# Optimization experiments

Hardware: AMD Instinct MI355X
Metric: run time of the kernel (lower is better)

The kernel has to match this reference:

```python
import jax, jax.numpy as jnp
import numpy as np

EPS = 1e-5

def setup_inputs() -> dict:
    key = jax.random.key(0)
    k1, k2 = jax.random.split(key)
    N, D = 8192, 256
    q_features = jax.random.normal(k1, (N, D), dtype=jnp.float32)
    g_features = jax.random.normal(k2, (N, D), dtype=jnp.float32)
    return {"q_features": q_features, "g_features": g_features}

def reference(q_features, g_features):
    # logits[i, j] = q_i . g_j ; original computes row i as g_features @ q_i
    logits = jnp.einsum('id,jd->ij', q_features, g_features)  # [N, N]
    # exp(l_ii)/sum_j exp(l_ij) == softmax row diagonal (stable form, same math)
    probs_diag = jnp.diagonal(jax.nn.softmax(logits, axis=-1))  # [N]
    loss = jnp.mean(-jnp.log(probs_diag + EPS))
    return loss
```

## Files before the change

kernel.cpp:

```cpp
#include <hip/hip_runtime.h>
#include <stdint.h>


#define LOG2E 1.44269504f
#define KOFF  92.3324826f

typedef __attribute__((ext_vector_type(4))) float f32x4;
typedef long long i64;

typedef __attribute__((address_space(1))) const uint32_t gu32;
typedef __attribute__((address_space(3))) uint32_t lu32;

__global__ __launch_bounds__(256) void k_cvt(const float* __restrict__ q,
                                             const float* __restrict__ g,
                                             char* __restrict__ qb,
                                             char* __restrict__ gb) {
    int o = blockIdx.x * 256 + threadIdx.x;
    const float* src = q;
    char* dst = qb;
    float sc = LOG2E;
    if (o >= 262144) { o -= 262144; src = g; dst = gb; sc = 1.0f; }
    int row = o >> 5, slot = o & 31;
    int ks = slot >> 2, quad = slot & 3;
    const float4* sp = (const float4*)(src + row * 256 + slot * 8);
    float4 a = sp[0], b = sp[1];
    uint32_t w0 = __builtin_amdgcn_cvt_pk_fp8_f32(a.x * sc, a.y * sc, 0, false);
    w0 = __builtin_amdgcn_cvt_pk_fp8_f32(a.z * sc, a.w * sc, w0, true);
    uint32_t w1 = __builtin_amdgcn_cvt_pk_fp8_f32(b.x * sc, b.y * sc, 0, false);
    w1 = __builtin_amdgcn_cvt_pk_fp8_f32(b.z * sc, b.w * sc, w1, true);
    int p = row >> 6, cf = (row >> 4) & 3, l15 = row & 15;
    uint2 wv; wv.x = w0; wv.y = w1;
    *(uint2*)(dst + (size_t)p * 16384 + (ks * 4 + cf) * 512 + (quad * 16 + l15) * 8) = wv;
}

__global__ __launch_bounds__(256, 2) void k_main(const char* __restrict__ qb,
                                                 const char* __restrict__ gb,
                                                 float* __restrict__ zpart,
                                                 float* __restrict__ diag) {
    __shared__ char lds[16384];
    const int tid  = threadIdx.x;
    const int wave = tid >> 6;
    const int lane = tid & 63;
    const int l15  = lane & 15;
    const int quad = lane >> 4;
    const int t    = blockIdx.x >> 5;
    const int cs   = blockIdx.x & 31;
    const int rowbase = t * 256 + wave * 64;

    i64 afrag[4][8];
    {
        const char* qp = qb + (size_t)(t * 4 + wave) * 16384 + lane * 8;
#pragma unroll
        for (int rg = 0; rg < 4; ++rg)
#pragma unroll
            for (int ks = 0; ks < 8; ++ks)
                afrag[rg][ks] = *(const i64*)(qp + ((ks * 4 + rg) << 9));
    }

    float zacc[4][4];
#pragma unroll
    for (int rg = 0; rg < 4; ++rg)
#pragma unroll
        for (int r = 0; r < 4; ++r) zacc[rg][r] = 0.f;

    const bool bd = (t == cs);

    for (int jt = 0; jt < 4; ++jt) {
        const char* gp = gb + (size_t)(cs * 4 + jt) * 16384;
#pragma unroll
        for (int i = 0; i < 4; ++i) {
            int c = wave * 4 + i;
            __builtin_amdgcn_global_load_lds(
                (gu32*)(gp + (c << 10) + (lane << 4)),
                (lu32*)(lds + (c << 10)), 16, 0, 0);
        }
        __syncthreads();

        const bool dg = bd && (jt == wave);
#pragma unroll
        for (int cf = 0; cf < 4; ++cf) {
            f32x4 acc[4];
#pragma unroll
            for (int rg = 0; rg < 4; ++rg)
                acc[rg] = (f32x4){-KOFF, -KOFF, -KOFF, -KOFF};
#pragma unroll
            for (int ks = 0; ks < 8; ++ks) {
                i64 b = *(const i64*)(lds + ((ks * 4 + cf) << 9) + lane * 8);
#pragma unroll
                for (int rg = 0; rg < 4; ++rg)
                    acc[rg] = __builtin_amdgcn_mfma_f32_16x16x32_fp8_fp8(
                        afrag[rg][ks], b, acc[rg], 0, 0, 0);
            }
#pragma unroll
            for (int rg = 0; rg < 4; ++rg)
#pragma unroll
                for (int r = 0; r < 4; ++r)
                    zacc[rg][r] += __builtin_amdgcn_exp2f(acc[rg][r]);
            if (dg) {
#pragma unroll
                for (int r = 0; r < 4; ++r)
                    if (quad * 4 + r == l15)
                        diag[rowbase + cf * 16 + l15] = acc[cf][r];
            }
        }
        __syncthreads();
    }

#pragma unroll
    for (int d = 1; d < 16; d <<= 1)
#pragma unroll
        for (int rg = 0; rg < 4; ++rg)
#pragma unroll
            for (int r = 0; r < 4; ++r)
                zacc[rg][r] += __shfl_xor(zacc[rg][r], d, 64);

    if (l15 == 0) {
#pragma unroll
        for (int rg = 0; rg < 4; ++rg)
#pragma unroll
            for (int r = 0; r < 4; ++r)
                zpart[(rowbase + rg * 16 + quad * 4 + r) * 32 + cs] = zacc[rg][r];
    }
}

__global__ __launch_bounds__(256) void k_fin1(const float* __restrict__ zpart,
                                              const float* __restrict__ diag,
                                              float* __restrict__ partial) {
    __shared__ float red[4];
    int r = blockIdx.x * 256 + threadIdx.x;
    const float4* z = (const float4*)(zpart + r * 32);
    float Z = 0.f;
#pragma unroll
    for (int i = 0; i < 8; ++i) {
        float4 a = z[i];
        Z += (a.x + a.y) + (a.z + a.w);
    }
    float p = __builtin_amdgcn_exp2f(diag[r]) / Z;
    float v = -logf(p + 1e-5f);
#pragma unroll
    for (int dd = 1; dd < 64; dd <<= 1) v += __shfl_xor(v, dd, 64);
    if ((threadIdx.x & 63) == 0) red[threadIdx.x >> 6] = v;
    __syncthreads();
    if (threadIdx.x == 0)
        partial[blockIdx.x] = (red[0] + red[1]) + (red[2] + red[3]);
}

__global__ void k_fin2(const float* __restrict__ partial, float* __restrict__ out) {
    float v = (threadIdx.x < 32) ? partial[threadIdx.x] : 0.f;
#pragma unroll
    for (int d = 1; d < 32; d <<= 1) v += __shfl_xor(v, d, 64);
    if (threadIdx.x == 0) out[0] = v * (1.f / 8192.f);
}

extern "C" void kernel_launch(void* const* d_in, const int* in_sizes, int n_in,
                              void* d_out, int out_size, void* d_ws, size_t ws_size,
                              hipStream_t stream) {
    const float* q = (const float*)d_in[0];
    const float* g = (const float*)d_in[1];
    char* ws = (char*)d_ws;
    char*  qb     = ws;
    char*  gb     = ws + (2u << 20);
    float* diag   = (float*)(ws + (4u << 20));
    float* zpart  = (float*)(ws + (4u << 20) + (32u << 10));
    float* partial= (float*)(ws + (4u << 20) + (1056u << 10));
    k_cvt <<<2048, 256, 0, stream>>>(q, g, qb, gb);
    k_main<<<1024, 256, 0, stream>>>(qb, gb, zpart, diag);
    k_fin1<<<32,   256, 0, stream>>>(zpart, diag, partial);
    k_fin2<<<1,     64, 0, stream>>>(partial, (float*)d_out);
    (void)in_sizes; (void)n_in; (void)out_size; (void)ws_size;
}
```

Baseline: 97.25 us.

## Switch to 16x16x128 scaled FP8 MFMA with repacked operand layout

Replaces the 16x16x32 FP8 MFMA with the gfx950 scaled 16x16x128 f8f6f4 MFMA using unit scales (0x7f). The conversion kernel's output layout changes so each lane loads 32 contiguous-K bytes as two 16-byte pieces, and LDS and A-fragment loads become 128-bit reads. This cuts MFMA instruction count by four and halves load instruction count per K. The risk is that the K ordering inside the new operand must match between the A and B sides, and that the wider vectors raise register pressure.

```diff
diff --git a/kernel.cpp b/kernel.cpp
--- a/kernel.cpp
+++ b/kernel.cpp
@@ -6,10 +6,18 @@
 #define KOFF  92.3324826f
 
 typedef __attribute__((ext_vector_type(4))) float f32x4;
-typedef long long i64;
+typedef __attribute__((ext_vector_type(4))) int   i32x4;
+typedef __attribute__((ext_vector_type(8))) int   i32x8;
 
 typedef __attribute__((address_space(1))) const uint32_t gu32;
 typedef __attribute__((address_space(3))) uint32_t lu32;
+
+static __device__ __forceinline__ i32x8 cat8(i32x4 lo, i32x4 hi) {
+    i32x8 r;
+    r[0] = lo[0]; r[1] = lo[1]; r[2] = lo[2]; r[3] = lo[3];
+    r[4] = hi[0]; r[5] = hi[1]; r[6] = hi[2]; r[7] = hi[3];
+    return r;
+}
 
 __global__ __launch_bounds__(256) void k_cvt(const float* __restrict__ q,
                                              const float* __restrict__ g,
@@ -21,7 +29,6 @@
     float sc = LOG2E;
     if (o >= 262144) { o -= 262144; src = g; dst = gb; sc = 1.0f; }
     int row = o >> 5, slot = o & 31;
-    int ks = slot >> 2, quad = slot & 3;
     const float4* sp = (const float4*)(src + row * 256 + slot * 8);
     float4 a = sp[0], b = sp[1];
     uint32_t w0 = __builtin_amdgcn_cvt_pk_fp8_f32(a.x * sc, a.y * sc, 0, false);
@@ -29,8 +36,13 @@
     uint32_t w1 = __builtin_amdgcn_cvt_pk_fp8_f32(b.x * sc, b.y * sc, 0, false);
     w1 = __builtin_amdgcn_cvt_pk_fp8_f32(b.z * sc, b.w * sc, w1, true);
     int p = row >> 6, cf = (row >> 4) & 3, l15 = row & 15;
+    int kb = slot >> 4;
+    int gi = slot & 15;
+    int quad = gi >> 2;
+    int j = gi & 3;
     uint2 wv; wv.x = w0; wv.y = w1;
-    *(uint2*)(dst + (size_t)p * 16384 + (ks * 4 + cf) * 512 + (quad * 16 + l15) * 8) = wv;
+    *(uint2*)(dst + (size_t)p * 16384 + ((kb * 4 + cf) << 11)
+              + ((j >> 1) << 10) + (quad * 16 + l15) * 16 + (j & 1) * 8) = wv;
 }
 
 __global__ __launch_bounds__(256, 2) void k_main(const char* __restrict__ qb,
@@ -47,14 +59,16 @@
     const int cs   = blockIdx.x & 31;
     const int rowbase = t * 256 + wave * 64;
 
-    i64 afrag[4][8];
+    i32x8 afrag[4][2];
     {
-        const char* qp = qb + (size_t)(t * 4 + wave) * 16384 + lane * 8;
+        const char* qp = qb + (size_t)(t * 4 + wave) * 16384 + lane * 16;
 #pragma unroll
         for (int rg = 0; rg < 4; ++rg)
 #pragma unroll
-            for (int ks = 0; ks < 8; ++ks)
-                afrag[rg][ks] = *(const i64*)(qp + ((ks * 4 + rg) << 9));
+            for (int kb = 0; kb < 2; ++kb) {
+                const char* tp = qp + ((kb * 4 + rg) << 11);
+                afrag[rg][kb] = cat8(*(const i32x4*)tp, *(const i32x4*)(tp + 1024));
+            }
     }
 
     float zacc[4][4];
@@ -84,12 +98,16 @@
             for (int rg = 0; rg < 4; ++rg)
                 acc[rg] = (f32x4){-KOFF, -KOFF, -KOFF, -KOFF};
 #pragma unroll
-            for (int ks = 0; ks < 8; ++ks) {
-                i64 b = *(const i64*)(lds + ((ks * 4 + cf) << 9) + lane * 8);
+            for (int kb = 0; kb < 2; ++kb) {
+                const char* bp = lds + ((kb * 4 + cf) << 11) + lane * 16;
+                i32x8 b = cat8(*(const i32x4*)bp, *(const i32x4*)(bp + 1024));
 #pragma unroll
                 for (int rg = 0; rg < 4; ++rg)
-                    acc[rg] = __builtin_amdgcn_mfma_f32_16x16x32_fp8_fp8(
-                        afrag[rg][ks], b, acc[rg], 0, 0, 0);
+                    acc[rg] = __builtin_amdgcn_mfma_scale_f32_16x16x128_f8f6f4(
+                        afrag[rg][kb], b, acc[rg],
+                        0, 0,
+                        0, 0x7f7f7f7f,
+                        0, 0x7f7f7f7f);
             }
 #pragma unroll
             for (int rg = 0; rg < 4; ++rg)
```

After: 268.2 us. 2.76x slower.
